# Performance work log

Measured on AMD Instinct MI355X. Metric: run time of the kernel, lower is better.

The kernel has to match this reference:

```python
import jax, jax.numpy as jnp
import numpy as np

EMB_DIM = 768
NUM_HEADS = 12
OUT_DIM = 768


def setup_inputs() -> dict:
    key = jax.random.key(0)
    k_x, k_q, k_k, k_v, k_o = jax.random.split(key, 5)
    B, N, D = 8, 1024, EMB_DIM
    s = 1.0 / np.sqrt(D)
    return {
        "x": jax.random.normal(k_x, (B, N, D), dtype=jnp.float32),
        # torch nn.Linear weights are stored [out_features, in_features]
        "Wq": jax.random.normal(k_q, (D, D), dtype=jnp.float32) * s,
        "Wk": jax.random.normal(k_k, (D, D), dtype=jnp.float32) * s,
        "Wv": jax.random.normal(k_v, (D, D), dtype=jnp.float32) * s,
        "Wo": jax.random.normal(k_o, (OUT_DIM, D), dtype=jnp.float32) * s,
    }


def _split_heads(t, H):
    # [B, N, D] -> [B*H, N, D//H]  (heads folded into batch, per einsum 'b i d')
    B, N, D = t.shape
    return t.reshape(B, N, H, D // H).transpose(0, 2, 1, 3).reshape(B * H, N, D // H)


def _merge_heads(t, B, H):
    BH, N, dh = t.shape
    return t.reshape(B, H, N, dh).transpose(0, 2, 1, 3).reshape(B, N, H * dh)


def reference(x, Wq, Wk, Wv, Wo):
    B, N, D = x.shape
    H = NUM_HEADS
    dh = D // H
    # q/k/v projections (torch Linear: y = x @ W.T, no bias)
    q = _split_heads(x @ Wq.T, H)
    k = _split_heads(x @ Wk.T, H)
    v = _split_heads(x @ Wv.T, H)
    scale = dh ** (-0.5)
    # dots: 'b i d , b j d -> b i j' -> full [B*H, N, N] score matrix
    dots = jnp.einsum('bid,bjd->bij', q, k) * scale
    attn = jax.nn.softmax(dots, axis=-1)
    # dropout p=0.0 -> identity
    # vect: 'b i d , b d j -> b i j' == attn @ v
    vect = jnp.einsum('bij,bjd->bid', attn, v)
    out = _merge_heads(vect, B, H) @ Wo.T
    return out
```

## Files before the change

kernel.cpp:

```cpp
#include <hip/hip_runtime.h>
#include <hip/hip_bf16.h>
#include <stdint.h>


typedef __bf16 bf16x8 __attribute__((ext_vector_type(8)));
typedef __bf16 bf16x4 __attribute__((ext_vector_type(4)));
typedef float f32x4 __attribute__((ext_vector_type(4)));

#define GAS __attribute__((address_space(1)))
#define LAS __attribute__((address_space(3)))

__device__ __forceinline__ void glds16(const short* gp, short* lp) {
  __builtin_amdgcn_global_load_lds((const GAS void*)gp, (LAS void*)lp, 16, 0, 0);
}

__device__ __forceinline__ float fast_exp2(float x) {
#if __has_builtin(__builtin_amdgcn_exp2f)
  return __builtin_amdgcn_exp2f(x);
#else
  return __expf(x * 0.6931471805599453f);
#endif
}

__device__ __forceinline__ short bfbits(float f) {
  __bf16 b = (__bf16)f;
  union { __bf16 b; short s; } cv; cv.b = b;
  return cv.s;
}

__device__ __forceinline__ void stage8_f32(const float* __restrict__ src, short* dst) {
  float4 f0 = ((const float4*)src)[0];
  float4 f1 = ((const float4*)src)[1];
  bf16x8 t;
  t[0] = (__bf16)f0.x; t[1] = (__bf16)f0.y; t[2] = (__bf16)f0.z; t[3] = (__bf16)f0.w;
  t[4] = (__bf16)f1.x; t[5] = (__bf16)f1.y; t[6] = (__bf16)f1.z; t[7] = (__bf16)f1.w;
  *(bf16x8*)dst = t;
}

__global__ __launch_bounds__(256) void convert_kernel(
    const float* __restrict__ x, const float* __restrict__ Wq,
    const float* __restrict__ Wk, const float* __restrict__ Wv,
    const float* __restrict__ Wo,
    short* __restrict__ xb, short* __restrict__ wqkv, short* __restrict__ wob) {
  int u0 = blockIdx.x * 1024 + threadIdx.x;
#pragma unroll
  for (int i = 0; i < 4; ++i) {
    int u = u0 + i * 256;
    const float* src; short* dst;
    if (u < 786432) { src = x + (size_t)u * 8; dst = xb + (size_t)u * 8; }
    else if (u < 1007616) {
      int r = u - 786432;
      int wsel = r / 73728, off = r % 73728;
      const float* W = (wsel == 0) ? Wq : (wsel == 1) ? Wk : Wv;
      src = W + (size_t)off * 8;
      dst = wqkv + (size_t)r * 8;
    } else {
      int r = u - 1007616;
      src = Wo + (size_t)r * 8; dst = wob + (size_t)r * 8;
    }
    stage8_f32(src, dst);
  }
}

__device__ __forceinline__ void stage_half(const short* __restrict__ g, short* l,
                                           int w, int lane) {
#pragma unroll
  for (int p = 0; p < 2; ++p) {
    int c = (w * 2 + p) * 64 + lane;
    int row = c >> 3;
    int cs = ((c & 7) ^ (row & 7)) * 8;
    glds16(g + (size_t)row * 768 + cs, l + c * 8);
  }
}

__device__ __forceinline__ void stage_b192(const short* __restrict__ g, short* l,
                                           int w, int lane) {
#pragma unroll
  for (int p = 0; p < 3; ++p) {
    int c = (w * 3 + p) * 64 + lane;
    int row = c >> 3;
    int cs = ((c & 7) ^ (row & 7)) * 8;
    glds16(g + (size_t)row * 768 + cs, l + c * 8);
  }
}

__device__ __forceinline__ void bar_fence() {
  asm volatile("" ::: "memory");
  __builtin_amdgcn_s_barrier();
  asm volatile("" ::: "memory");
}

__device__ __forceinline__ void load_a8(const short* base, int wr, int l16, int quad,
                                        bf16x8 (&fa)[4][2]) {
#pragma unroll
  for (int mf = 0; mf < 4; ++mf)
#pragma unroll
    for (int kk = 0; kk < 2; ++kk) {
      int row = wr * 64 + mf * 16 + l16;
      fa[mf][kk] = *(const bf16x8*)&base[row * 64 + ((((kk << 2) + quad) ^ (row & 7)) << 3)];
    }
}

__device__ __forceinline__ void load_b4(const short* base, int rbase, int l16, int quad,
                                        bf16x8 (&fb)[2][2]) {
#pragma unroll
  for (int nf = 0; nf < 2; ++nf)
#pragma unroll
    for (int kk = 0; kk < 2; ++kk) {
      int row = rbase + nf * 16 + l16;
      fb[nf][kk] = *(const bf16x8*)&base[row * 64 + ((((kk << 2) + quad) ^ (row & 7)) << 3)];
    }
}

__device__ __forceinline__ void load_b2(const short* base, int rbase, int l16, int quad,
                                        bf16x8 (&fb)[2]) {
#pragma unroll
  for (int kk = 0; kk < 2; ++kk) {
    int row = rbase + l16;
    fb[kk] = *(const bf16x8*)&base[row * 64 + ((((kk << 2) + quad) ^ (row & 7)) << 3)];
  }
}

__device__ __forceinline__ void mma16(const bf16x8 (&fa)[4][2], const bf16x8 (&fb)[2][2],
                                      f32x4 (&acc)[4][4], int nf0) {
  __builtin_amdgcn_s_setprio(1);
#pragma unroll
  for (int kk = 0; kk < 2; ++kk)
#pragma unroll
    for (int mf = 0; mf < 4; ++mf)
#pragma unroll
      for (int nf = 0; nf < 2; ++nf)
        acc[mf][nf0 + nf] = __builtin_amdgcn_mfma_f32_16x16x32_bf16(
            fa[mf][kk], fb[nf][kk], acc[mf][nf0 + nf], 0, 0, 0);
  __builtin_amdgcn_s_setprio(0);
}

__device__ __forceinline__ void mma16o(const bf16x8 (&fa)[4][2], const bf16x8 (&fb)[2][2],
                                       f32x4 (&acc)[4][3]) {
  __builtin_amdgcn_s_setprio(1);
#pragma unroll
  for (int kk = 0; kk < 2; ++kk)
#pragma unroll
    for (int mf = 0; mf < 4; ++mf)
#pragma unroll
      for (int nf = 0; nf < 2; ++nf)
        acc[mf][nf] = __builtin_amdgcn_mfma_f32_16x16x32_bf16(
            fa[mf][kk], fb[nf][kk], acc[mf][nf], 0, 0, 0);
  __builtin_amdgcn_s_setprio(0);
}

__device__ __forceinline__ void mma8o(const bf16x8 (&fa)[4][2], const bf16x8 (&fb)[2],
                                      f32x4 (&acc)[4][3]) {
  __builtin_amdgcn_s_setprio(1);
#pragma unroll
  for (int kk = 0; kk < 2; ++kk)
#pragma unroll
    for (int mf = 0; mf < 4; ++mf)
      acc[mf][2] = __builtin_amdgcn_mfma_f32_16x16x32_bf16(
          fa[mf][kk], fb[kk], acc[mf][2], 0, 0, 0);
  __builtin_amdgcn_s_setprio(0);
}

__global__ __launch_bounds__(512, 4) void gemm_qkv(
    const short* __restrict__ xb, const short* __restrict__ wqkv,
    short* __restrict__ q, short* __restrict__ k, short* __restrict__ vt) {
  const int lin = blockIdx.x;
  const int xcd = lin & 7, grp = lin >> 3;
  const int by = grp >> 3;
  const int bx = xcd * 8 + (grp & 7);
  const int m0 = bx * 128;
  const int n0g = by * 256;
  const int tid = threadIdx.x;
  const int w = tid >> 6, lane = tid & 63, l16 = lane & 15, quad = lane >> 4;
  const int wr = w >> 2, wc = w & 3;

  __shared__ short sA[8192];
  __shared__ short sB[16384];

  const short* Asrc = xb + (size_t)m0 * 768;
  const short* Bsrc = wqkv + (size_t)n0g * 768;

  f32x4 acc[4][4];
#pragma unroll
  for (int i = 0; i < 4; ++i)
#pragma unroll
    for (int j = 0; j < 4; ++j) acc[i][j] = (f32x4){0.f, 0.f, 0.f, 0.f};

  const int bh = wc >> 1;
  const int rb0 = (wc & 1) * 64;

  for (int t = 0; t < 12; ++t) {
    __syncthreads();
    stage_half(Asrc + (size_t)t * 64, sA, w, lane);
    stage_half(Bsrc + (size_t)t * 64, sB, w, lane);
    stage_half(Bsrc + 98304 + (size_t)t * 64, &sB[8192], w, lane);
    __syncthreads();
    bf16x8 fa[4][2], fb0[2][2], fb1[2][2];
    load_a8(sA, wr, l16, quad, fa);
    load_b4(&sB[bh * 8192], rb0, l16, quad, fb0);
    mma16(fa, fb0, acc, 0);
    load_b4(&sB[bh * 8192], rb0 + 32, l16, quad, fb1);
    mma16(fa, fb1, acc, 2);
  }

  const int wsel = by / 3;
  const int nl0 = (by % 3) * 256 + wc * 64;
  if (wsel == 2) {
#pragma unroll
    for (int mf = 0; mf < 4; ++mf)
#pragma unroll
      for (int nf = 0; nf < 4; ++nf) {
        int token = m0 + wr * 64 + mf * 16 + quad * 4;
        int nl = nl0 + nf * 16 + l16;
        int bhh = (token >> 10) * 12 + (nl >> 6);
        int jt = (token >> 7) & 7;
        int fb = (wr * 2 + (mf >> 1)) * 4 + nf;
        short tmp[4];
#pragma unroll
        for (int r = 0; r < 4; ++r) tmp[r] = bfbits(acc[mf][nf][r]);
        *(uint2*)(vt + (size_t)bhh * 65536 + jt * 8192 + fb * 512 +
                  (l16 + 16 * quad) * 8 + (mf & 1) * 4) = *(const uint2*)tmp;
      }
  } else {
    short* C = wsel ? k : q;
    const float sc = wsel ? 1.0f : 0.1803368801111244f;
#pragma unroll
    for (int mf = 0; mf < 4; ++mf)
#pragma unroll
      for (int nf = 0; nf < 4; ++nf)
#pragma unroll
        for (int r = 0; r < 4; ++r) {
          int row = m0 + wr * 64 + mf * 16 + quad * 4 + r;
          int nl = nl0 + nf * 16 + l16;
          C[(size_t)row * 768 + nl] = bfbits(acc[mf][nf][r] * sc);
        }
  }
}

__device__ __forceinline__ void attn_stage_k(const short* __restrict__ kb, int j0,
                                             short* sK, int w, int lane) {
#pragma unroll
  for (int p = 0; p < 4; ++p) {
    int lin = (w * 4 + p) * 64 + lane;
    int row = lin >> 3;
    int cs = ((lin & 7) ^ (row & 7)) * 8;
    glds16(kb + (size_t)(j0 + row) * 768 + cs, &sK[lin * 8]);
  }
}

__global__ __launch_bounds__(256, 3) void attn_kernel(
    const short* __restrict__ q, const short* __restrict__ k,
    const short* __restrict__ vt, short* __restrict__ vect) {
  const int bh = blockIdx.x % 96;
  const int qt = blockIdx.x / 96;
  const int b = bh / 12, h = bh % 12;
  const int m0 = qt * 128;
  const int tid = threadIdx.x;
  const int w = tid >> 6, lane = tid & 63, l16 = lane & 15, quad = lane >> 4;

  __shared__ short sK[128 * 64];

  const size_t base = (size_t)b * 786432 + (size_t)h * 64;
  const short* kb = k + base;
  const short* vb = vt + (size_t)bh * 65536;

#pragma unroll
  for (int p = 0; p < 4; ++p) {
    int lin = (w * 4 + p) * 64 + lane;
    int row = lin >> 3;
    int cs = ((lin & 7) ^ (row & 7)) * 8;
    glds16(q + base + (size_t)(m0 + row) * 768 + cs, &sK[lin * 8]);
  }
  asm volatile("s_waitcnt vmcnt(0)" ::: "memory");
  bar_fence();
  bf16x8 bq[2][2];
#pragma unroll
  for (int g = 0; g < 2; ++g)
#pragma unroll
    for (int kk = 0; kk < 2; ++kk) {
      int row = g * 64 + w * 16 + l16;
      bq[g][kk] = *(const bf16x8*)&sK[row * 64 + (((kk * 4 + quad) ^ (row & 7)) << 3)];
    }
  asm volatile("s_waitcnt lgkmcnt(0)" ::: "memory");
  __builtin_amdgcn_sched_barrier(0);
  bar_fence();

  attn_stage_k(kb, 0, sK, w, lane);

  f32x4 l4[2];
  l4[0] = (f32x4){0.f, 0.f, 0.f, 0.f};
  l4[1] = (f32x4){0.f, 0.f, 0.f, 0.f};
  f32x4 oacc[2][4];
#pragma unroll
  for (int g = 0; g < 2; ++g)
#pragma unroll
    for (int td = 0; td < 4; ++td) oacc[g][td] = (f32x4){0.f, 0.f, 0.f, 0.f};

  for (int jt = 0; jt < 8; ++jt) {
    asm volatile("s_waitcnt vmcnt(0)" ::: "memory");
    bar_fence();

    bf16x4 pb[2][2][4];
#pragma unroll
    for (int jh = 0; jh < 2; ++jh) {
      f32x4 s[2][4];
#pragma unroll
      for (int g = 0; g < 2; ++g)
#pragma unroll
        for (int ti = 0; ti < 4; ++ti) s[g][ti] = (f32x4){0.f, 0.f, 0.f, 0.f};
      __builtin_amdgcn_s_setprio(1);
#pragma unroll
      for (int kk = 0; kk < 2; ++kk)
#pragma unroll
        for (int ti = 0; ti < 4; ++ti) {
          int row = jh * 64 + ti * 16 + l16;
          bf16x8 a = *(const bf16x8*)&sK[row * 64 + (((kk * 4 + quad) ^ (row & 7)) << 3)];
          s[0][ti] = __builtin_amdgcn_mfma_f32_16x16x32_bf16(a, bq[0][kk], s[0][ti], 0, 0, 0);
          s[1][ti] = __builtin_amdgcn_mfma_f32_16x16x32_bf16(a, bq[1][kk], s[1][ti], 0, 0, 0);
        }
      __builtin_amdgcn_s_setprio(0);
#pragma unroll
      for (int g = 0; g < 2; ++g)
#pragma unroll
        for (int ti = 0; ti < 4; ++ti) {
          f32x4 e;
          e[0] = fast_exp2(s[g][ti][0]);
          e[1] = fast_exp2(s[g][ti][1]);
          e[2] = fast_exp2(s[g][ti][2]);
          e[3] = fast_exp2(s[g][ti][3]);
          l4[g] += e;
          bf16x4 tb;
          tb[0] = (__bf16)e[0]; tb[1] = (__bf16)e[1];
          tb[2] = (__bf16)e[2]; tb[3] = (__bf16)e[3];
          pb[jh][g][ti] = tb;
        }
    }
    asm volatile("s_waitcnt lgkmcnt(0)" ::: "memory");
    __builtin_amdgcn_sched_barrier(0);
    bar_fence();

    const short* vj = vb + (size_t)jt * 8192;
#pragma unroll
    for (int jh = 0; jh < 2; ++jh) {
      bf16x8 av[2][4];
#pragma unroll
      for (int t2 = 0; t2 < 2; ++t2)
#pragma unroll
        for (int td = 0; td < 4; ++td)
          av[t2][td] = *(const bf16x8*)(vj + ((jh * 2 + t2) * 4 + td) * 512 + lane * 8);
      if (jh == 0 && jt < 7) attn_stage_k(kb, (jt + 1) * 128, sK, w, lane);
      __builtin_amdgcn_s_setprio(1);
#pragma unroll
      for (int t2 = 0; t2 < 2; ++t2) {
        union { bf16x4 hh[2]; bf16x8 v; } bp0, bp1;
        bp0.hh[0] = pb[jh][0][2 * t2];
        bp0.hh[1] = pb[jh][0][2 * t2 + 1];
        bp1.hh[0] = pb[jh][1][2 * t2];
        bp1.hh[1] = pb[jh][1][2 * t2 + 1];
#pragma unroll
        for (int td = 0; td < 4; ++td) {
          oacc[0][td] = __builtin_amdgcn_mfma_f32_16x16x32_bf16(av[t2][td], bp0.v, oacc[0][td], 0, 0, 0);
          oacc[1][td] = __builtin_amdgcn_mfma_f32_16x16x32_bf16(av[t2][td], bp1.v, oacc[1][td], 0, 0, 0);
        }
      }
      __builtin_amdgcn_s_setprio(0);
    }
  }

#pragma unroll
  for (int g = 0; g < 2; ++g) {
    float l = (l4[g][0] + l4[g][1]) + (l4[g][2] + l4[g][3]);
    l += __shfl_xor(l, 16);
    l += __shfl_xor(l, 32);
    float inv = 1.0f / l;
    int i_tok = m0 + g * 64 + w * 16 + l16;
#pragma unroll
    for (int td = 0; td < 4; ++td) {
      short tmp[4];
#pragma unroll
      for (int r = 0; r < 4; ++r) tmp[r] = bfbits(oacc[g][td][r] * inv);
      *(uint2*)(vect + base + (size_t)i_tok * 768 + td * 16 + quad * 4) = *(const uint2*)tmp;
    }
  }
}

__global__ __launch_bounds__(512, 2) void gemm_out(
    const short* __restrict__ vect, const short* __restrict__ wob,
    float* __restrict__ out) {
  const int lin = blockIdx.x;
  const int xcd = lin & 7, grp = lin >> 3;
  const int by = grp >> 3;
  const int bx = xcd * 8 + (grp & 7);
  const int m0 = bx * 128;
  const int n0g = by * 192;
  const int tid = threadIdx.x;
  const int w = tid >> 6, lane = tid & 63, l16 = lane & 15, quad = lane >> 4;
  const int wr = w >> 2, wc = w & 3;

  __shared__ short lds[3][20480];

  const short* Asrc = vect + (size_t)m0 * 768;
  const short* Bsrc = wob + (size_t)n0g * 768;

  f32x4 acc[4][3];
#pragma unroll
  for (int i = 0; i < 4; ++i)
#pragma unroll
    for (int j = 0; j < 3; ++j) acc[i][j] = (f32x4){0.f, 0.f, 0.f, 0.f};

  stage_half(Asrc, &lds[0][0], w, lane);
  stage_b192(Bsrc, &lds[0][8192], w, lane);
  stage_half(Asrc + 64, &lds[1][0], w, lane);
  stage_b192(Bsrc + 64, &lds[1][8192], w, lane);
  asm volatile("s_waitcnt vmcnt(5)" ::: "memory");
  bar_fence();

  const int rb0 = wc * 48;
  bf16x8 fa[4][2], fb01[2][2], fb2[2];

#pragma unroll
  for (int t = 0; t < 12; ++t) {
    const int buf = t % 3, nb = (t + 2) % 3;
    const bool pf = (t < 10);
    const short* A = &lds[buf][0];
    const short* Bb = &lds[buf][8192];

    load_a8(A, wr, l16, quad, fa);
    load_b4(Bb, rb0, l16, quad, fb01);
    if (pf) stage_half(Asrc + (size_t)(t + 2) * 64, &lds[nb][0], w, lane);
    bar_fence();
    __builtin_amdgcn_sched_barrier(0);
    mma16o(fa, fb01, acc);
    __builtin_amdgcn_sched_barrier(0);
    bar_fence();

    load_b2(Bb, rb0 + 32, l16, quad, fb2);
    if (pf) {
      stage_b192(Bsrc + (size_t)(t + 2) * 64, &lds[nb][8192], w, lane);
      asm volatile("s_waitcnt vmcnt(5)" ::: "memory");
    } else if (t == 10) {
      asm volatile("s_waitcnt vmcnt(0)" ::: "memory");
    }
    bar_fence();
    __builtin_amdgcn_sched_barrier(0);
    mma8o(fa, fb2, acc);
    __builtin_amdgcn_sched_barrier(0);
    bar_fence();
  }

#pragma unroll
  for (int mf = 0; mf < 4; ++mf)
#pragma unroll
    for (int nf = 0; nf < 3; ++nf)
#pragma unroll
      for (int r = 0; r < 4; ++r) {
        int row = m0 + wr * 64 + mf * 16 + quad * 4 + r;
        int col = n0g + wc * 48 + nf * 16 + l16;
        out[(size_t)row * 768 + col] = acc[mf][nf][r];
      }
}

extern "C" void kernel_launch(void* const* d_in, const int* in_sizes, int n_in,
                              void* d_out, int out_size, void* d_ws, size_t ws_size,
                              hipStream_t stream) {
  const float* x  = (const float*)d_in[0];
  const float* Wq = (const float*)d_in[1];
  const float* Wk = (const float*)d_in[2];
  const float* Wv = (const float*)d_in[3];
  const float* Wo = (const float*)d_in[4];
  float* out = (float*)d_out;

  const size_t MN = (size_t)8192 * 768;
  short* q    = (short*)d_ws;
  short* k    = q + MN;
  short* vt   = k + MN;
  short* vect = q;
  short* wob  = vt + MN;

  short* xb   = (short*)d_out;
  short* wqkv = xb + MN;

  convert_kernel<<<1056, 256, 0, stream>>>(x, Wq, Wk, Wv, Wo, xb, wqkv, wob);
  gemm_qkv<<<576, 512, 0, stream>>>(xb, wqkv, q, k, vt);
  attn_kernel<<<768, 256, 0, stream>>>(q, k, vt, vect);
  gemm_out<<<256, 512, 0, stream>>>(vect, wob, out);
}
```

Baseline: 188.1 us.

## Process 512 queries per attention block with double-buffered K and V in LDS

Each attention block now handles four 128-row query chunks (512 queries) instead of one, so every K/V tile it loads is reused across four times as many queries. K and V tiles are staged into double-buffered LDS, with the next tile prefetched while the current one is consumed, and V is read from LDS instead of straight from global memory. Blocks are mapped so each XCD handles one batch. Cost: the grid shrinks from 768 to 192 blocks with launch_bounds occupancy 1, and the register footprint (4x accumulators, Q fragments and K fragments) grows a lot, which risks spills and leaves too few waves to hide latency.

```diff
diff --git a/kernel.cpp b/kernel.cpp
--- a/kernel.cpp
+++ b/kernel.cpp
@@ -248,140 +248,160 @@
   }
 }
 
-__global__ __launch_bounds__(256, 3) void attn_kernel(
+__device__ __forceinline__ void attn_stage_v(const short* __restrict__ vb, int jt,
+                                             short* sVt, int w, int lane) {
+#pragma unroll
+  for (int p = 0; p < 4; ++p) {
+    int c = (w * 4 + p) * 64 + lane;
+    glds16(vb + (size_t)jt * 8192 + (size_t)c * 8, &sVt[c * 8]);
+  }
+}
+
+__global__ __launch_bounds__(256, 1) void attn_kernel(
     const short* __restrict__ q, const short* __restrict__ k,
     const short* __restrict__ vt, short* __restrict__ vect) {
-  const int bh = blockIdx.x % 96;
-  const int qt = blockIdx.x / 96;
-  const int b = bh / 12, h = bh % 12;
-  const int m0 = qt * 128;
+  const int lin = blockIdx.x;
+  const int xcd = lin & 7, g8 = lin >> 3;
+  const int bhl = g8 >> 1, half = g8 & 1;
+  const int b = xcd, h = bhl;
+  const int bh = b * 12 + h;
+  const int m0b = half * 512;
   const int tid = threadIdx.x;
   const int w = tid >> 6, lane = tid & 63, l16 = lane & 15, quad = lane >> 4;
 
-  __shared__ short sK[128 * 64];
+  __shared__ short sK[2][128 * 64];
+  __shared__ short sVt[2][64 * 128];
 
   const size_t base = (size_t)b * 786432 + (size_t)h * 64;
   const short* kb = k + base;
   const short* vb = vt + (size_t)bh * 65536;
 
-#pragma unroll
-  for (int p = 0; p < 4; ++p) {
-    int lin = (w * 4 + p) * 64 + lane;
-    int row = lin >> 3;
-    int cs = ((lin & 7) ^ (row & 7)) * 8;
-    glds16(q + base + (size_t)(m0 + row) * 768 + cs, &sK[lin * 8]);
-  }
-  asm volatile("s_waitcnt vmcnt(0)" ::: "memory");
-  bar_fence();
-  bf16x8 bq[2][2];
-#pragma unroll
-  for (int g = 0; g < 2; ++g)
-#pragma unroll
-    for (int kk = 0; kk < 2; ++kk) {
-      int row = g * 64 + w * 16 + l16;
-      bq[g][kk] = *(const bf16x8*)&sK[row * 64 + (((kk * 4 + quad) ^ (row & 7)) << 3)];
-    }
-  asm volatile("s_waitcnt lgkmcnt(0)" ::: "memory");
-  __builtin_amdgcn_sched_barrier(0);
-  bar_fence();
-
-  attn_stage_k(kb, 0, sK, w, lane);
-
-  f32x4 l4[2];
-  l4[0] = (f32x4){0.f, 0.f, 0.f, 0.f};
-  l4[1] = (f32x4){0.f, 0.f, 0.f, 0.f};
-  f32x4 oacc[2][4];
-#pragma unroll
-  for (int g = 0; g < 2; ++g)
-#pragma unroll
-    for (int td = 0; td < 4; ++td) oacc[g][td] = (f32x4){0.f, 0.f, 0.f, 0.f};
+  bf16x8 bq[4][2][2];
+#pragma unroll
+  for (int c = 0; c < 4; ++c)
+#pragma unroll
+    for (int g = 0; g < 2; ++g)
+#pragma unroll
+      for (int kk = 0; kk < 2; ++kk) {
+        int row = m0b + c * 128 + g * 64 + w * 16 + l16;
+        bq[c][g][kk] =
+            *(const bf16x8*)(q + base + (size_t)row * 768 + (kk * 4 + quad) * 8);
+      }
+  attn_stage_k(kb, 0, sK[0], w, lane);
+  attn_stage_v(vb, 0, sVt[0], w, lane);
+
+  f32x4 l4[4][2];
+  f32x4 oacc[4][2][4];
+#pragma unroll
+  for (int c = 0; c < 4; ++c)
+#pragma unroll
+    for (int g = 0; g < 2; ++g) {
+      l4[c][g] = (f32x4){0.f, 0.f, 0.f, 0.f};
+#pragma unroll
+      for (int td = 0; td < 4; ++td) oacc[c][g][td] = (f32x4){0.f, 0.f, 0.f, 0.f};
+    }
 
   for (int jt = 0; jt < 8; ++jt) {
+    const int buf = jt & 1;
     asm volatile("s_waitcnt vmcnt(0)" ::: "memory");
     bar_fence();
 
-    bf16x4 pb[2][2][4];
-#pragma unroll
-    for (int jh = 0; jh < 2; ++jh) {
-      f32x4 s[2][4];
-#pragma unroll
-      for (int g = 0; g < 2; ++g)
-#pragma unroll
-        for (int ti = 0; ti < 4; ++ti) s[g][ti] = (f32x4){0.f, 0.f, 0.f, 0.f};
-      __builtin_amdgcn_s_setprio(1);
+    bf16x8 ka[2][2][4];
+#pragma unroll
+    for (int jh = 0; jh < 2; ++jh)
 #pragma unroll
       for (int kk = 0; kk < 2; ++kk)
 #pragma unroll
         for (int ti = 0; ti < 4; ++ti) {
           int row = jh * 64 + ti * 16 + l16;
-          bf16x8 a = *(const bf16x8*)&sK[row * 64 + (((kk * 4 + quad) ^ (row & 7)) << 3)];
-          s[0][ti] = __builtin_amdgcn_mfma_f32_16x16x32_bf16(a, bq[0][kk], s[0][ti], 0, 0, 0);
-          s[1][ti] = __builtin_amdgcn_mfma_f32_16x16x32_bf16(a, bq[1][kk], s[1][ti], 0, 0, 0);
+          ka[jh][kk][ti] =
+              *(const bf16x8*)&sK[buf][row * 64 + (((kk * 4 + quad) ^ (row & 7)) << 3)];
+        }
+    if (jt < 7) {
+      attn_stage_k(kb, (jt + 1) * 128, sK[buf ^ 1], w, lane);
+      attn_stage_v(vb, jt + 1, sVt[buf ^ 1], w, lane);
+    }
+
+#pragma unroll
+    for (int c = 0; c < 4; ++c) {
+      bf16x4 pb[2][2][4];
+#pragma unroll
+      for (int jh = 0; jh < 2; ++jh) {
+        f32x4 s[2][4];
+#pragma unroll
+        for (int g = 0; g < 2; ++g)
+#pragma unroll
+          for (int ti = 0; ti < 4; ++ti) s[g][ti] = (f32x4){0.f, 0.f, 0.f, 0.f};
+        __builtin_amdgcn_s_setprio(1);
+#pragma unroll
+        for (int kk = 0; kk < 2; ++kk)
+#pragma unroll
+          for (int ti = 0; ti < 4; ++ti) {
+            s[0][ti] = __builtin_amdgcn_mfma_f32_16x16x32_bf16(
+                ka[jh][kk][ti], bq[c][0][kk], s[0][ti], 0, 0, 0);
+            s[1][ti] = __builtin_amdgcn_mfma_f32_16x16x32_bf16(
+                ka[jh][kk][ti], bq[c][1][kk], s[1][ti], 0, 0, 0);
+          }
+        __builtin_amdgcn_s_setprio(0);
+#pragma unroll
+        for (int g = 0; g < 2; ++g)
+#pragma unroll
+          for (int ti = 0; ti < 4; ++ti) {
+            f32x4 e;
+            e[0] = fast_exp2(s[g][ti][0]);
+            e[1] = fast_exp2(s[g][ti][1]);
+            e[2] = fast_exp2(s[g][ti][2]);
+            e[3] = fast_exp2(s[g][ti][3]);
+            l4[c][g] += e;
+            bf16x4 tb;
+            tb[0] = (__bf16)e[0]; tb[1] = (__bf16)e[1];
+            tb[2] = (__bf16)e[2]; tb[3] = (__bf16)e[3];
+            pb[jh][g][ti] = tb;
+          }
+      }
+
+      __builtin_amdgcn_s_setprio(1);
+#pragma unroll
+      for (int jh = 0; jh < 2; ++jh)
+#pragma unroll
+        for (int t2 = 0; t2 < 2; ++t2) {
+          union { bf16x4 hh[2]; bf16x8 v; } bp0, bp1;
+          bp0.hh[0] = pb[jh][0][2 * t2];
+          bp0.hh[1] = pb[jh][0][2 * t2 + 1];
+          bp1.hh[0] = pb[jh][1][2 * t2];
+          bp1.hh[1] = pb[jh][1][2 * t2 + 1];
+          const int fbi = (jh * 2 + t2) * 4;
+#pragma unroll
+          for (int td = 0; td < 4; ++td) {
+            bf16x8 av = *(const bf16x8*)&sVt[buf][(fbi + td) * 512 + lane * 8];
+            oacc[c][0][td] = __builtin_amdgcn_mfma_f32_16x16x32_bf16(
+                av, bp0.v, oacc[c][0][td], 0, 0, 0);
+            oacc[c][1][td] = __builtin_amdgcn_mfma_f32_16x16x32_bf16(
+                av, bp1.v, oacc[c][1][td], 0, 0, 0);
+          }
         }
       __builtin_amdgcn_s_setprio(0);
-#pragma unroll
-      for (int g = 0; g < 2; ++g)
-#pragma unroll
-        for (int ti = 0; ti < 4; ++ti) {
-          f32x4 e;
-          e[0] = fast_exp2(s[g][ti][0]);
-          e[1] = fast_exp2(s[g][ti][1]);
-          e[2] = fast_exp2(s[g][ti][2]);
-          e[3] = fast_exp2(s[g][ti][3]);
-          l4[g] += e;
-          bf16x4 tb;
-          tb[0] = (__bf16)e[0]; tb[1] = (__bf16)e[1];
-          tb[2] = (__bf16)e[2]; tb[3] = (__bf16)e[3];
-          pb[jh][g][ti] = tb;
-        }
-    }
-    asm volatile("s_waitcnt lgkmcnt(0)" ::: "memory");
-    __builtin_amdgcn_sched_barrier(0);
-    bar_fence();
-
-    const short* vj = vb + (size_t)jt * 8192;
-#pragma unroll
-    for (int jh = 0; jh < 2; ++jh) {
-      bf16x8 av[2][4];
-#pragma unroll
-      for (int t2 = 0; t2 < 2; ++t2)
-#pragma unroll
-        for (int td = 0; td < 4; ++td)
-          av[t2][td] = *(const bf16x8*)(vj + ((jh * 2 + t2) * 4 + td) * 512 + lane * 8);
-      if (jh == 0 && jt < 7) attn_stage_k(kb, (jt + 1) * 128, sK, w, lane);
-      __builtin_amdgcn_s_setprio(1);
-#pragma unroll
-      for (int t2 = 0; t2 < 2; ++t2) {
-        union { bf16x4 hh[2]; bf16x8 v; } bp0, bp1;
-        bp0.hh[0] = pb[jh][0][2 * t2];
-        bp0.hh[1] = pb[jh][0][2 * t2 + 1];
-        bp1.hh[0] = pb[jh][1][2 * t2];
-        bp1.hh[1] = pb[jh][1][2 * t2 + 1];
-#pragma unroll
-        for (int td = 0; td < 4; ++td) {
-          oacc[0][td] = __builtin_amdgcn_mfma_f32_16x16x32_bf16(av[t2][td], bp0.v, oacc[0][td], 0, 0, 0);
-          oacc[1][td] = __builtin_amdgcn_mfma_f32_16x16x32_bf16(av[t2][td], bp1.v, oacc[1][td], 0, 0, 0);
-        }
+    }
+  }
+
+#pragma unroll
+  for (int c = 0; c < 4; ++c)
+#pragma unroll
+    for (int g = 0; g < 2; ++g) {
+      float l = (l4[c][g][0] + l4[c][g][1]) + (l4[c][g][2] + l4[c][g][3]);
+      l += __shfl_xor(l, 16);
+      l += __shfl_xor(l, 32);
+      float inv = 1.0f / l;
+      int i_tok = m0b + c * 128 + g * 64 + w * 16 + l16;
+#pragma unroll
+      for (int td = 0; td < 4; ++td) {
+        short tmp[4];
+#pragma unroll
+        for (int r = 0; r < 4; ++r) tmp[r] = bfbits(oacc[c][g][td][r] * inv);
+        *(uint2*)(vect + base + (size_t)i_tok * 768 + td * 16 + quad * 4) =
+            *(const uint2*)tmp;
       }
-      __builtin_amdgcn_s_setprio(0);
-    }
-  }
-
-#pragma unroll
-  for (int g = 0; g < 2; ++g) {
-    float l = (l4[g][0] + l4[g][1]) + (l4[g][2] + l4[g][3]);
-    l += __shfl_xor(l, 16);
-    l += __shfl_xor(l, 32);
-    float inv = 1.0f / l;
-    int i_tok = m0 + g * 64 + w * 16 + l16;
-#pragma unroll
-    for (int td = 0; td < 4; ++td) {
-      short tmp[4];
-#pragma unroll
-      for (int r = 0; r < 4; ++r) tmp[r] = bfbits(oacc[g][td][r] * inv);
-      *(uint2*)(vect + base + (size_t)i_tok * 768 + td * 16 + quad * 4) = *(const uint2*)tmp;
-    }
-  }
+    }
 }
 
 __global__ __launch_bounds__(512, 2) void gemm_out(
@@ -482,6 +502,6 @@
 
   convert_kernel<<<1056, 256, 0, stream>>>(x, Wq, Wk, Wv, Wo, xb, wqkv, wob);
   gemm_qkv<<<576, 512, 0, stream>>>(xb, wqkv, q, k, vt);
-  attn_kernel<<<768, 256, 0, stream>>>(q, k, vt, vect);
+  attn_kernel<<<192, 256, 0, stream>>>(q, k, vt, vect);
   gemm_out<<<256, 512, 0, stream>>>(vect, wob, out);
 }
```

Result: faster. 183.9 us (-2.3%).
